# Kernel tuning notes

Hardware: AMD Instinct MI355X
Metric: run time of the kernel (lower is better)

Reference implementation:

```python
import jax, jax.numpy as jnp
import numpy as np

NUM_CLASSES = 100000
FEAT_DIM = 128
BATCH = 1024
CLAMP_MIN = 1e-12
CLAMP_MAX = 1e12


def setup_inputs() -> dict:
    key = jax.random.key(0)
    k1, k2, k3 = jax.random.split(key, 3)
    input_x = jax.random.normal(k1, (BATCH, FEAT_DIM), dtype=jnp.float32)
    input_label = jax.random.randint(k2, (BATCH,), 0, NUM_CLASSES, dtype=jnp.int64)
    # learned parameter: class centers, initialized ~N(0,1) as in the module
    centers = jax.random.normal(k3, (NUM_CLASSES, FEAT_DIM), dtype=jnp.float32)
    return {"input_x": input_x, "input_label": input_label, "centers": centers}


def reference(input_x, input_label, centers):
    # distmat[b, c] = ||x_b||^2 + ||center_c||^2 - 2 <x_b, center_c>   -> [B, C]
    x_sq = jnp.sum(input_x * input_x, axis=1, keepdims=True)          # [B, 1]
    c_sq = jnp.sum(centers * centers, axis=1)[None, :]                # [1, C]
    distmat = x_sq + c_sq - 2.0 * (input_x @ centers.T)               # [B, C]
    # mask selects the true-class column per sample
    mask = (input_label[:, None] == jnp.arange(NUM_CLASSES)[None, :]).astype(distmat.dtype)
    dist = distmat * mask
    # NOTE: faithful to the original — clamp is applied AFTER masking, so every
    # masked-off zero entry clamps up to 1e-12 and contributes to the sum.
    loss = jnp.clip(dist, CLAMP_MIN, CLAMP_MAX).sum() / BATCH
    return loss
```

## Files before the change

kernel.cpp:

```cpp
#include <hip/hip_runtime.h>


#define BATCH 1024
#define FEAT_DIM 128
#define NUM_CLASSES 100000

__global__ void center_row_dist_kernel(const float* __restrict__ x,
                                       const int* __restrict__ label,
                                       const float* __restrict__ centers,
                                       float* __restrict__ row_out) {
    const int gtid      = blockIdx.x * blockDim.x + threadIdx.x;
    const int wave      = gtid >> 6;
    const int lane      = threadIdx.x & 63;
    const int num_waves = (gridDim.x * blockDim.x) >> 6;

    for (int row = wave; row < BATCH; row += num_waves) {
        const int lbl = label[row];
        const float2 xv = *reinterpret_cast<const float2*>(x + (size_t)row * FEAT_DIM + lane * 2);
        const float2 cv = *reinterpret_cast<const float2*>(centers + (size_t)lbl * FEAT_DIM + lane * 2);
        const float d0 = xv.x - cv.x;
        const float d1 = xv.y - cv.y;
        float s = d0 * d0 + d1 * d1;

        #pragma unroll
        for (int off = 32; off > 0; off >>= 1)
            s += __shfl_xor(s, off, 64);

        if (lane == 0) {
            s = fminf(fmaxf(s, 1e-12f), 1e12f);
            row_out[row] = s;
        }
    }
}

__global__ void center_loss_reduce_kernel(const float* __restrict__ row_vals,
                                          float* __restrict__ out) {
    __shared__ float sm[256];
    const int tid = threadIdx.x;
    float s = row_vals[tid] + row_vals[tid + 256] + row_vals[tid + 512] + row_vals[tid + 768];
    sm[tid] = s;
    __syncthreads();
    #pragma unroll
    for (int off = 128; off >= 1; off >>= 1) {
        if (tid < off) sm[tid] += sm[tid + off];
        __syncthreads();
    }
    if (tid == 0) {
        const float masked_contrib = (float)(NUM_CLASSES - 1) * 1e-12f;
        out[0] = sm[0] / (float)BATCH + masked_contrib;
    }
}

extern "C" void kernel_launch(void* const* d_in, const int* in_sizes, int n_in,
                              void* d_out, int out_size, void* d_ws, size_t ws_size,
                              hipStream_t stream) {
    const float* x       = (const float*)d_in[0];
    const int*   label   = (const int*)d_in[1];
    const float* centers = (const float*)d_in[2];
    float*       out     = (float*)d_out;
    float*       ws      = (float*)d_ws;

    center_row_dist_kernel<<<64, 256, 0, stream>>>(x, label, centers, ws);
    center_loss_reduce_kernel<<<1, 256, 0, stream>>>(ws, out);
}
```

Baseline: 11.67 us.

## Fuse row distance and reduction into one cooperative kernel with grid sync

Replaces the two-kernel pipeline with a single cooperative launch. Each wave accumulates its four rows locally, each block writes one partial sum, and after a grid-wide sync block 0 reduces the 64 partials with wave shuffles. This removes the second kernel launch and the 1024-entry intermediate buffer. In exchange it depends on cooperative launch and grid.sync, which add their own launch and barrier overhead.

```diff
diff --git a/kernel.cpp b/kernel.cpp
--- a/kernel.cpp
+++ b/kernel.cpp
@@ -1,53 +1,58 @@
 #include <hip/hip_runtime.h>
+#include <hip/hip_cooperative_groups.h>
+
+namespace cg = cooperative_groups;
 
 
 #define BATCH 1024
 #define FEAT_DIM 128
 #define NUM_CLASSES 100000
+#define NBLK 64
+#define NTHR 256
 
-__global__ void center_row_dist_kernel(const float* __restrict__ x,
-                                       const int* __restrict__ label,
-                                       const float* __restrict__ centers,
-                                       float* __restrict__ row_out) {
-    const int gtid      = blockIdx.x * blockDim.x + threadIdx.x;
-    const int wave      = gtid >> 6;
-    const int lane      = threadIdx.x & 63;
-    const int num_waves = (gridDim.x * blockDim.x) >> 6;
+__global__ void center_loss_coop(const float* __restrict__ x,
+                                 const int* __restrict__ label,
+                                 const float* __restrict__ centers,
+                                 float* __restrict__ out,
+                                 float* __restrict__ partials) {
+    cg::grid_group grid = cg::this_grid();
 
-    for (int row = wave; row < BATCH; row += num_waves) {
+    const int lane  = threadIdx.x & 63;
+    const int wid   = threadIdx.x >> 6;
+    const int gwave = blockIdx.x * 4 + wid;
+
+    float wsum = 0.f;
+    #pragma unroll
+    for (int r = 0; r < 4; ++r) {
+        const int row = gwave + 256 * r;
         const int lbl = label[row];
         const float2 xv = *reinterpret_cast<const float2*>(x + (size_t)row * FEAT_DIM + lane * 2);
         const float2 cv = *reinterpret_cast<const float2*>(centers + (size_t)lbl * FEAT_DIM + lane * 2);
         const float d0 = xv.x - cv.x;
         const float d1 = xv.y - cv.y;
         float s = d0 * d0 + d1 * d1;
-
         #pragma unroll
         for (int off = 32; off > 0; off >>= 1)
             s += __shfl_xor(s, off, 64);
+        wsum += fminf(fmaxf(s, 1e-12f), 1e12f);
+    }
 
-        if (lane == 0) {
-            s = fminf(fmaxf(s, 1e-12f), 1e12f);
-            row_out[row] = s;
+    __shared__ float sm[4];
+    if (lane == 0) sm[wid] = wsum;
+    __syncthreads();
+    if (threadIdx.x == 0)
+        partials[blockIdx.x] = sm[0] + sm[1] + sm[2] + sm[3];
+
+    grid.sync();
+
+    if (blockIdx.x == 0 && threadIdx.x < 64) {
+        float v = partials[threadIdx.x];
+        #pragma unroll
+        for (int off = 32; off > 0; off >>= 1)
+            v += __shfl_xor(v, off, 64);
+        if (threadIdx.x == 0) {
+            out[0] = v / (float)BATCH + (float)(NUM_CLASSES - 1) * 1e-12f;
         }
-    }
-}
-
-__global__ void center_loss_reduce_kernel(const float* __restrict__ row_vals,
-                                          float* __restrict__ out) {
-    __shared__ float sm[256];
-    const int tid = threadIdx.x;
-    float s = row_vals[tid] + row_vals[tid + 256] + row_vals[tid + 512] + row_vals[tid + 768];
-    sm[tid] = s;
-    __syncthreads();
-    #pragma unroll
-    for (int off = 128; off >= 1; off >>= 1) {
-        if (tid < off) sm[tid] += sm[tid + off];
-        __syncthreads();
-    }
-    if (tid == 0) {
-        const float masked_contrib = (float)(NUM_CLASSES - 1) * 1e-12f;
-        out[0] = sm[0] / (float)BATCH + masked_contrib;
     }
 }
 
@@ -60,6 +65,7 @@
     float*       out     = (float*)d_out;
     float*       ws      = (float*)d_ws;
 
-    center_row_dist_kernel<<<64, 256, 0, stream>>>(x, label, centers, ws);
-    center_loss_reduce_kernel<<<1, 256, 0, stream>>>(ws, out);
+    void* args[] = {(void*)&x, (void*)&label, (void*)&centers, (void*)&out, (void*)&ws};
+    hipLaunchCooperativeKernel((void*)center_loss_coop, dim3(NBLK), dim3(NTHR),
+                               args, 0, stream);
 }
```

Result: slower. 32.29 us (+176.6%).
